# Kernel tuning notes

Measured on AMD Instinct MI355X. Metric: run time of the kernel, lower is better.

## Reference

```python
import jax, jax.numpy as jnp
import numpy as np
import math

B, N, K, C_IN, C_OUT = 2, 16384, 16, 128, 128


def _gather_neighbors(x, idx):
    # x: [B, N, C], idx: [B, N, K] -> [B, N, K, C]
    return jax.vmap(lambda xb, ib: xb[ib])(x, idx)


def setup_inputs() -> dict:
    key = jax.random.key(0)
    k1, k2, k3 = jax.random.split(key, 3)
    x = jax.random.normal(k1, (B, N, C_IN), dtype=jnp.float32)
    edge_index = jax.random.randint(k2, (2, B, N, K), 0, N, dtype=jnp.int64)
    W = jax.random.normal(k3, (C_OUT, C_IN), dtype=jnp.float32) * (1.0 / math.sqrt(C_IN))
    b = jnp.zeros((C_OUT,), dtype=jnp.float32)
    return {"x": x, "edge_index": edge_index, "W": W, "b": b}


def reference(x, edge_index, W, b):
    # x: [B, N, C]; edge_index: [2, B, N, K]
    x_i = _gather_neighbors(x, edge_index[1])  # [B, N, K, C] (centers)
    x_j = _gather_neighbors(x, edge_index[0])  # [B, N, K, C] (neighbors)
    scale = 1.0 / math.sqrt(x_i.shape[-1])
    scores = jnp.einsum('bnkc,bnjc->bnkj', x_i, x_j) * scale  # [B, N, K, K]
    p_attn = jax.nn.softmax(scores, axis=-1)
    h_k = jnp.einsum('bnkj,bnjc->bnkc', p_attn, x_j).sum(axis=-2)  # [B, N, C]
    y = (x + h_k) @ W.T + b  # Linear(in_channels -> out_channels)
    return jax.nn.relu(y)
```

## Files before the change

### kernel.cpp

```cpp
#include <hip/hip_runtime.h>
#include <hip/hip_bf16.h>
#include <math.h>

#define BB 2
#define NN 16384
#define KK 16
#define CC 128
#define COUT 128
#define NODES (BB * NN)

typedef __attribute__((ext_vector_type(8))) short bf16x8;
typedef __attribute__((ext_vector_type(4))) float f32x4;

__device__ __forceinline__ bf16x8 cvt8(f32x4 a, f32x4 b) {
    union { bf16x8 v; __hip_bfloat162 h[4]; } u;
    u.h[0] = __float22bfloat162_rn(make_float2(a[0], a[1]));
    u.h[1] = __float22bfloat162_rn(make_float2(a[2], a[3]));
    u.h[2] = __float22bfloat162_rn(make_float2(b[0], b[1]));
    u.h[3] = __float22bfloat162_rn(make_float2(b[2], b[3]));
    return u.v;
}

template <int CTRL>
__device__ __forceinline__ float rot_add(float v) {
    int r = __builtin_amdgcn_update_dpp(0, __float_as_int(v), CTRL, 0xF, 0xF, true);
    return v + __int_as_float(r);
}
__device__ __forceinline__ float row16_sum(float v) {
    v = rot_add<0x128>(v); v = rot_add<0x124>(v);
    v = rot_add<0x122>(v); v = rot_add<0x121>(v);
    return v;
}
__device__ __forceinline__ float row16_sum4(float v) {
    v = rot_add<0x128>(v); v = rot_add<0x124>(v);
    return v;
}

__global__ __launch_bounds__(256) void cast_x(
    const float* __restrict__ x, __hip_bfloat16* __restrict__ xh)
{
    const int i = blockIdx.x * 256 + threadIdx.x;
    const f32x4* p = (const f32x4*)(x + (size_t)i * 8);
    f32x4 a = p[0], b = p[1];
    *(bf16x8*)(xh + (size_t)i * 8) = cvt8(a, b);
}

__device__ __forceinline__ float col_weight(f32x4 acc) {
    const float scale = 0.08838834764831843f;
    float w = 0.f;
    #pragma unroll
    for (int i = 0; i < 4; ++i) {
        float e = __expf(acc[i] * scale);
        float s = row16_sum(e);
        w += e * __builtin_amdgcn_rcpf(s);
    }
    w += __shfl_xor(w, 16, 64);
    w += __shfl_xor(w, 32, 64);
    return w;
}

__device__ __forceinline__ float2 reduce_h(const bf16x8* bfr, float wj,
                                           float* hb, int m, int q, int lane) {
    #pragma unroll
    for (int s = 0; s < 4; ++s) {
        union { bf16x8 v; unsigned short u[8]; } ub;
        ub.v = bfr[s];
        float f[8];
        #pragma unroll
        for (int e = 0; e < 8; ++e) {
            f[e] = __uint_as_float((unsigned)ub.u[e] << 16) * wj;
            f[e] = row16_sum4(f[e]);
        }
        if (m < 4) {
            f32x4 lo = {f[0], f[1], f[2], f[3]};
            f32x4 hi = {f[4], f[5], f[6], f[7]};
            *(f32x4*)&hb[m * 132 + 32 * s + 8 * q]     = lo;
            *(f32x4*)&hb[m * 132 + 32 * s + 8 * q + 4] = hi;
        }
    }
    float hx = 0.f, hy = 0.f;
    #pragma unroll
    for (int r = 0; r < 4; ++r) {
        float2 v = *(const float2*)&hb[r * 132 + 2 * lane];
        hx += v.x; hy += v.y;
    }
    return make_float2(hx, hy);
}

__global__ __launch_bounds__(256) void attn_phase(
    const float* __restrict__ x,
    const __hip_bfloat16* __restrict__ xh,
    const int* __restrict__ edge,
    __hip_bfloat16* __restrict__ z)
{
    __shared__ float hbuf[4][2][4 * 132];

    const int t = threadIdx.x;
    const int wv = t >> 6;
    const int lane = t & 63;
    const int m = lane & 15;
    const int q = lane >> 4;
    const int node0 = blockIdx.x * 8 + wv * 2;
    const int b = node0 >> 14;
    const __hip_bfloat16* xbh = xh + (size_t)b * (size_t)(NN * CC);

    const size_t e0 = (size_t)node0 * KK + m;
    const int j0 = edge[e0];
    const int j1 = edge[e0 + KK];
    const int i0 = edge[(size_t)(NODES * KK) + e0];
    const int i1 = edge[(size_t)(NODES * KK) + e0 + KK];

    const __hip_bfloat16* pi0 = xbh + (size_t)i0 * CC + q * 8;
    const __hip_bfloat16* pj0 = xbh + (size_t)j0 * CC + q * 8;
    const __hip_bfloat16* pi1 = xbh + (size_t)i1 * CC + q * 8;
    const __hip_bfloat16* pj1 = xbh + (size_t)j1 * CC + q * 8;
    bf16x8 a0[4], b0[4], a1[4], b1[4];
    #pragma unroll
    for (int s = 0; s < 4; ++s) {
        a0[s] = *(const bf16x8*)(pi0 + 32 * s);
        b0[s] = *(const bf16x8*)(pj0 + 32 * s);
        a1[s] = *(const bf16x8*)(pi1 + 32 * s);
        b1[s] = *(const bf16x8*)(pj1 + 32 * s);
    }

    f32x4 acc0 = {0.f, 0.f, 0.f, 0.f};
    f32x4 acc1 = {0.f, 0.f, 0.f, 0.f};
    #pragma unroll
    for (int s = 0; s < 4; ++s) {
        acc0 = __builtin_amdgcn_mfma_f32_16x16x32_bf16(a0[s], b0[s], acc0, 0, 0, 0);
        acc1 = __builtin_amdgcn_mfma_f32_16x16x32_bf16(a1[s], b1[s], acc1, 0, 0, 0);
    }

    const float w0 = col_weight(acc0);
    const float w1 = col_weight(acc1);

    float2 h0 = reduce_h(b0, w0, &hbuf[wv][0][0], m, q, lane);
    float2 h1 = reduce_h(b1, w1, &hbuf[wv][1][0], m, q, lane);

    const float* xb = x + (size_t)b * (size_t)(NN * CC);
    const int n0 = node0 & (NN - 1);
    float2 xc0 = *(const float2*)(xb + (size_t)n0 * CC + 2 * lane);
    float2 xc1 = *(const float2*)(xb + (size_t)(n0 + 1) * CC + 2 * lane);
    __hip_bfloat162 z0 = __float22bfloat162_rn(make_float2(xc0.x + h0.x, xc0.y + h0.y));
    __hip_bfloat162 z1 = __float22bfloat162_rn(make_float2(xc1.x + h1.x, xc1.y + h1.y));
    *(__hip_bfloat162*)(z + (size_t)node0 * CC + 2 * lane) = z0;
    *(__hip_bfloat162*)(z + (size_t)(node0 + 1) * CC + 2 * lane) = z1;
}

__global__ __launch_bounds__(256, 4) void linear_relu(
    const __hip_bfloat16* __restrict__ z,
    const float* __restrict__ W,
    const float* __restrict__ bias,
    float* __restrict__ out)
{
    const int t = threadIdx.x;
    const int lane = t & 63;
    const int wid = blockIdx.x * 4 + (t >> 6);
    const int ntile = wid & 7;
    const int m0 = wid >> 3;
    const int nm = lane & 15;
    const int nq = lane >> 4;

    const float* wp = W + (size_t)(ntile * 16 + nm) * CC + nq * 8;
    bf16x8 bfr[4];
    #pragma unroll
    for (int s = 0; s < 4; ++s) {
        f32x4 w0 = *(const f32x4*)(wp + 32 * s);
        f32x4 w1 = *(const f32x4*)(wp + 32 * s + 4);
        bfr[s] = cvt8(w0, w1);
    }
    const float bv = bias[ntile * 16 + nm];

    #pragma unroll
    for (int it = 0; it < 4; ++it) {
        const int mt = m0 + it * 512;
        const __hip_bfloat16* zp = z + (size_t)(mt * 16 + nm) * CC + nq * 8;
        bf16x8 afr[4];
        #pragma unroll
        for (int s = 0; s < 4; ++s)
            afr[s] = *(const bf16x8*)(zp + 32 * s);
        f32x4 acc = {0.f, 0.f, 0.f, 0.f};
        #pragma unroll
        for (int s = 0; s < 4; ++s)
            acc = __builtin_amdgcn_mfma_f32_16x16x32_bf16(afr[s], bfr[s], acc, 0, 0, 0);
        float* op = out + (size_t)(mt * 16 + nq * 4) * COUT + ntile * 16 + nm;
        #pragma unroll
        for (int i = 0; i < 4; ++i)
            op[(size_t)i * COUT] = fmaxf(acc[i] + bv, 0.f);
    }
}

extern "C" void kernel_launch(void* const* d_in, const int* in_sizes, int n_in,
                              void* d_out, int out_size, void* d_ws, size_t ws_size,
                              hipStream_t stream) {
    const float* x    = (const float*)d_in[0];
    const int*   edge = (const int*)d_in[1];
    const float* W    = (const float*)d_in[2];
    const float* bias = (const float*)d_in[3];
    float* out = (float*)d_out;
    __hip_bfloat16* z  = (__hip_bfloat16*)d_ws;
    __hip_bfloat16* xh = (__hip_bfloat16*)d_ws + (size_t)NODES * CC;

    cast_x<<<(NODES * CC) / (256 * 8), 256, 0, stream>>>(x, xh);
    attn_phase<<<NODES / 8, 256, 0, stream>>>(x, xh, edge, z);
    linear_relu<<<1024, 256, 0, stream>>>(z, W, bias, out);
}
```

Baseline: 123.0 us.

## Fuse attention aggregation with linear+ReLU through LDS staging

Merges the attention kernel and the linear/ReLU kernel into one 512-thread block kernel. Each block handles 16 nodes, stages the bf16 z rows in padded shared memory, and then each of the 8 waves computes a 16-column output tile with MFMA. This removes the global z write and re-read and one kernel launch. In exchange, every block reloads and converts W, and the residual now reads the bf16 copy of x instead of fp32. Nontemporal load and store hints are also added for the streaming edge, x and output traffic.

```diff
diff --git a/kernel.cpp b/kernel.cpp
--- a/kernel.cpp
+++ b/kernel.cpp
@@ -8,6 +8,7 @@
 #define CC 128
 #define COUT 128
 #define NODES (BB * NN)
+#define ZP 144
 
 typedef __attribute__((ext_vector_type(8))) short bf16x8;
 typedef __attribute__((ext_vector_type(4))) float f32x4;
@@ -41,7 +42,8 @@
 {
     const int i = blockIdx.x * 256 + threadIdx.x;
     const f32x4* p = (const f32x4*)(x + (size_t)i * 8);
-    f32x4 a = p[0], b = p[1];
+    f32x4 a = __builtin_nontemporal_load(p);
+    f32x4 b = __builtin_nontemporal_load(p + 1);
     *(bf16x8*)(xh + (size_t)i * 8) = cvt8(a, b);
 }
 
@@ -87,28 +89,30 @@
     return make_float2(hx, hy);
 }
 
-__global__ __launch_bounds__(256) void attn_phase(
-    const float* __restrict__ x,
+__global__ __launch_bounds__(512) void attn_fused(
     const __hip_bfloat16* __restrict__ xh,
     const int* __restrict__ edge,
-    __hip_bfloat16* __restrict__ z)
+    const float* __restrict__ W,
+    const float* __restrict__ bias,
+    float* __restrict__ out)
 {
-    __shared__ float hbuf[4][2][4 * 132];
+    __shared__ float hbuf[8][4 * 132];
+    __shared__ __hip_bfloat16 z_lds[16 * ZP];
 
     const int t = threadIdx.x;
     const int wv = t >> 6;
     const int lane = t & 63;
     const int m = lane & 15;
     const int q = lane >> 4;
-    const int node0 = blockIdx.x * 8 + wv * 2;
+    const int node0 = blockIdx.x * 16 + wv * 2;
     const int b = node0 >> 14;
     const __hip_bfloat16* xbh = xh + (size_t)b * (size_t)(NN * CC);
 
     const size_t e0 = (size_t)node0 * KK + m;
-    const int j0 = edge[e0];
-    const int j1 = edge[e0 + KK];
-    const int i0 = edge[(size_t)(NODES * KK) + e0];
-    const int i1 = edge[(size_t)(NODES * KK) + e0 + KK];
+    const int j0 = __builtin_nontemporal_load(edge + e0);
+    const int j1 = __builtin_nontemporal_load(edge + e0 + KK);
+    const int i0 = __builtin_nontemporal_load(edge + (size_t)(NODES * KK) + e0);
+    const int i1 = __builtin_nontemporal_load(edge + (size_t)(NODES * KK) + e0 + KK);
 
     const __hip_bfloat16* pi0 = xbh + (size_t)i0 * CC + q * 8;
     const __hip_bfloat16* pj0 = xbh + (size_t)j0 * CC + q * 8;
@@ -134,60 +138,43 @@
     const float w0 = col_weight(acc0);
     const float w1 = col_weight(acc1);
 
-    float2 h0 = reduce_h(b0, w0, &hbuf[wv][0][0], m, q, lane);
-    float2 h1 = reduce_h(b1, w1, &hbuf[wv][1][0], m, q, lane);
+    float2 h0 = reduce_h(b0, w0, &hbuf[wv][0], m, q, lane);
+    float2 h1 = reduce_h(b1, w1, &hbuf[wv][0], m, q, lane);
 
-    const float* xb = x + (size_t)b * (size_t)(NN * CC);
     const int n0 = node0 & (NN - 1);
-    float2 xc0 = *(const float2*)(xb + (size_t)n0 * CC + 2 * lane);
-    float2 xc1 = *(const float2*)(xb + (size_t)(n0 + 1) * CC + 2 * lane);
-    __hip_bfloat162 z0 = __float22bfloat162_rn(make_float2(xc0.x + h0.x, xc0.y + h0.y));
-    __hip_bfloat162 z1 = __float22bfloat162_rn(make_float2(xc1.x + h1.x, xc1.y + h1.y));
-    *(__hip_bfloat162*)(z + (size_t)node0 * CC + 2 * lane) = z0;
-    *(__hip_bfloat162*)(z + (size_t)(node0 + 1) * CC + 2 * lane) = z1;
-}
+    __hip_bfloat162 rx0 = *(const __hip_bfloat162*)(xbh + (size_t)n0 * CC + 2 * lane);
+    __hip_bfloat162 rx1 = *(const __hip_bfloat162*)(xbh + (size_t)(n0 + 1) * CC + 2 * lane);
+    float2 xc0 = __bfloat1622float2(rx0);
+    float2 xc1 = __bfloat1622float2(rx1);
+    const int slot = wv * 2;
+    *(__hip_bfloat162*)&z_lds[slot * ZP + 2 * lane] =
+        __float22bfloat162_rn(make_float2(xc0.x + h0.x, xc0.y + h0.y));
+    *(__hip_bfloat162*)&z_lds[(slot + 1) * ZP + 2 * lane] =
+        __float22bfloat162_rn(make_float2(xc1.x + h1.x, xc1.y + h1.y));
 
-__global__ __launch_bounds__(256, 4) void linear_relu(
-    const __hip_bfloat16* __restrict__ z,
-    const float* __restrict__ W,
-    const float* __restrict__ bias,
-    float* __restrict__ out)
-{
-    const int t = threadIdx.x;
-    const int lane = t & 63;
-    const int wid = blockIdx.x * 4 + (t >> 6);
-    const int ntile = wid & 7;
-    const int m0 = wid >> 3;
-    const int nm = lane & 15;
-    const int nq = lane >> 4;
+    __syncthreads();
 
-    const float* wp = W + (size_t)(ntile * 16 + nm) * CC + nq * 8;
-    bf16x8 bfr[4];
+    bf16x8 afr[4], wfr[4];
+    #pragma unroll
+    for (int s = 0; s < 4; ++s)
+        afr[s] = *(const bf16x8*)&z_lds[m * ZP + s * 32 + q * 8];
+    const float* wrow = W + (size_t)(wv * 16 + m) * CC + q * 8;
     #pragma unroll
     for (int s = 0; s < 4; ++s) {
-        f32x4 w0 = *(const f32x4*)(wp + 32 * s);
-        f32x4 w1 = *(const f32x4*)(wp + 32 * s + 4);
-        bfr[s] = cvt8(w0, w1);
+        f32x4 wa = *(const f32x4*)(wrow + 32 * s);
+        f32x4 wb = *(const f32x4*)(wrow + 32 * s + 4);
+        wfr[s] = cvt8(wa, wb);
     }
-    const float bv = bias[ntile * 16 + nm];
+    f32x4 yacc = {0.f, 0.f, 0.f, 0.f};
+    #pragma unroll
+    for (int s = 0; s < 4; ++s)
+        yacc = __builtin_amdgcn_mfma_f32_16x16x32_bf16(afr[s], wfr[s], yacc, 0, 0, 0);
 
+    const float bv = bias[wv * 16 + m];
+    float* op = out + (size_t)(blockIdx.x * 16 + q * 4) * COUT + wv * 16 + m;
     #pragma unroll
-    for (int it = 0; it < 4; ++it) {
-        const int mt = m0 + it * 512;
-        const __hip_bfloat16* zp = z + (size_t)(mt * 16 + nm) * CC + nq * 8;
-        bf16x8 afr[4];
-        #pragma unroll
-        for (int s = 0; s < 4; ++s)
-            afr[s] = *(const bf16x8*)(zp + 32 * s);
-        f32x4 acc = {0.f, 0.f, 0.f, 0.f};
-        #pragma unroll
-        for (int s = 0; s < 4; ++s)
-            acc = __builtin_amdgcn_mfma_f32_16x16x32_bf16(afr[s], bfr[s], acc, 0, 0, 0);
-        float* op = out + (size_t)(mt * 16 + nq * 4) * COUT + ntile * 16 + nm;
-        #pragma unroll
-        for (int i = 0; i < 4; ++i)
-            op[(size_t)i * COUT] = fmaxf(acc[i] + bv, 0.f);
-    }
+    for (int i = 0; i < 4; ++i)
+        __builtin_nontemporal_store(fmaxf(yacc[i] + bv, 0.f), op + (size_t)i * COUT);
 }
 
 extern "C" void kernel_launch(void* const* d_in, const int* in_sizes, int n_in,
@@ -198,10 +185,8 @@
     const float* W    = (const float*)d_in[2];
     const float* bias = (const float*)d_in[3];
     float* out = (float*)d_out;
-    __hip_bfloat16* z  = (__hip_bfloat16*)d_ws;
-    __hip_bfloat16* xh = (__hip_bfloat16*)d_ws + (size_t)NODES * CC;
+    __hip_bfloat16* xh = (__hip_bfloat16*)d_ws;
 
     cast_x<<<(NODES * CC) / (256 * 8), 256, 0, stream>>>(x, xh);
-    attn_phase<<<NODES / 8, 256, 0, stream>>>(x, xh, edge, z);
-    linear_relu<<<1024, 256, 0, stream>>>(z, W, bias, out);
+    attn_fused<<<NODES / 16, 512, 0, stream>>>(xh, edge, W, bias, out);
 }
```

After: 124.7 us. No clear change (+1.3%).
